# Kernel optimization log

Hardware: AMD Instinct MI355X
Metric: run time of the kernel (lower is better)

The kernel has to match this reference:

```python
import jax, jax.numpy as jnp
import numpy as np

N_NODES = 100000
N_EDGES = 1600000
NODE_DIM = 128
EDGE_DIM = 32
HIDDEN_DIM = 256


def _linear_params(key, fan_in, fan_out):
    kw, kb = jax.random.split(key)
    bound = 1.0 / np.sqrt(fan_in)
    W = jax.random.uniform(kw, (fan_in, fan_out), minval=-bound, maxval=bound, dtype=jnp.float32)
    b = jax.random.uniform(kb, (fan_out,), minval=-bound, maxval=bound, dtype=jnp.float32)
    return W, b


def setup_inputs() -> dict:
    key = jax.random.key(0)
    ks = jax.random.split(key, 8)
    x = jax.random.normal(ks[0], (N_NODES, NODE_DIM), dtype=jnp.float32)
    edge_index = jax.random.randint(ks[1], (2, N_EDGES), 0, N_NODES, dtype=jnp.int64)
    edge_attr = jax.random.normal(ks[2], (N_EDGES, EDGE_DIM), dtype=jnp.float32)
    congestion = jax.random.uniform(ks[3], (N_NODES,), dtype=jnp.float32)
    msg_in = 2 * NODE_DIM + EDGE_DIM + 1
    mW1, mb1 = _linear_params(ks[4], msg_in, HIDDEN_DIM)
    mW2, mb2 = _linear_params(ks[5], HIDDEN_DIM, NODE_DIM)
    uW1, ub1 = _linear_params(ks[6], 2 * NODE_DIM, HIDDEN_DIM)
    uW2, ub2 = _linear_params(ks[7], HIDDEN_DIM, NODE_DIM)
    return {
        "x": x, "edge_index": edge_index, "edge_attr": edge_attr, "congestion": congestion,
        "mW1": mW1, "mb1": mb1, "mW2": mW2, "mb2": mb2,
        "uW1": uW1, "ub1": ub1, "uW2": uW2, "ub2": ub2,
    }


def reference(x, edge_index, edge_attr, congestion, mW1, mb1, mW2, mb2, uW1, ub1, uW2, ub2):
    src, dst = edge_index[0], edge_index[1]
    # gather node features and src congestion, concat along feature dim  [E, 2D+edge_dim+1]
    msg_in = jnp.concatenate(
        [x[src], x[dst], edge_attr, congestion[src][:, None]], axis=-1)
    h = jax.nn.relu(msg_in @ mW1 + mb1)          # [E, hidden]
    messages = h @ mW2 + mb2                     # [E, node_dim]
    # scatter_add messages into destination nodes  [N, node_dim]
    aggregated = jax.ops.segment_sum(messages, dst, num_segments=x.shape[0])
    upd_in = jnp.concatenate([x, aggregated], axis=-1)  # [N, 2*node_dim]
    h2 = jax.nn.relu(upd_in @ uW1 + ub1)
    x_new = h2 @ uW2 + ub2                       # [N, node_dim]
    return x_new
```

## Files before the change

kernel.cpp:

```cpp
#include <hip/hip_runtime.h>

#define E_TOTAL 1600000
#define NN 100000
#define D 128
#define ED 32
#define H 256

typedef __attribute__((ext_vector_type(8))) short s16x8;
typedef __attribute__((ext_vector_type(4))) short s16x4;
typedef __attribute__((ext_vector_type(4))) float f32x4;

#define MFMA(a, b, c) __builtin_amdgcn_mfma_f32_16x16x32_bf16((a), (b), (c), 0, 0, 0)

__device__ __forceinline__ short f2bf(float f) {
    unsigned u = __builtin_bit_cast(unsigned, f);
    u += 0x7fffu + ((u >> 16) & 1u);
    return (short)(u >> 16);
}
__device__ __forceinline__ float bf2f(short s) {
    return __builtin_bit_cast(float, ((unsigned)(unsigned short)s) << 16);
}

__device__ __forceinline__ void gll16(const void* g, void* l) {
    __builtin_amdgcn_global_load_lds(
        (const __attribute__((address_space(1))) void*)g,
        (__attribute__((address_space(3))) void*)l, 16, 0, 0);
}

__device__ __forceinline__ void swz_one(const float* __restrict__ W,
                                        short* __restrict__ out,
                                        int K, int N, int idx) {
    int j    = idx & 7;
    int lane = (idx >> 3) & 63;
    int rest = idx >> 9;
    int NT   = N >> 4;
    int nt   = rest % NT;
    int t    = rest / NT;
    int k    = t * 32 + (lane >> 4) * 8 + j;
    int col  = nt * 16 + (lane & 15);
    out[idx] = f2bf((k < K) ? W[k * N + col] : 0.f);
}

__global__ void k_prep(const float* __restrict__ x, short* __restrict__ xb,
                       const int* __restrict__ ei, int* __restrict__ cnt,
                       const float* __restrict__ mW1, short* __restrict__ W1s,
                       const float* __restrict__ mW2, short* __restrict__ W2s,
                       const float* __restrict__ uW1, short* __restrict__ U1s,
                       const float* __restrict__ uW2, short* __restrict__ U2s) {
    const int b = blockIdx.x;
    if (b < 12500) {
        int i = (b * 256 + threadIdx.x) * 4;
        if (i >= NN * D) return;
        f32x4 v = *(const f32x4*)(x + i);
        s16x4 o;
        o[0] = f2bf(v[0]); o[1] = f2bf(v[1]); o[2] = f2bf(v[2]); o[3] = f2bf(v[3]);
        *(s16x4*)(xb + i) = o;
    } else if (b < 18750) {
        int e = (b - 12500) * 256 + threadIdx.x;
        if (e < E_TOTAL) atomicAdd(&cnt[ei[E_TOTAL + e]], 1);
    } else {
        int idx = (b - 18750) * 256 + threadIdx.x;
        if (idx < 81920) { swz_one(mW1, W1s, 289, 256, idx); return; }
        idx -= 81920;
        if (idx < 32768) { swz_one(mW2, W2s, 256, 128, idx); return; }
        idx -= 32768;
        if (idx < 65536) { swz_one(uW1, U1s, 256, 256, idx); return; }
        idx -= 65536;
        if (idx < 32768) { swz_one(uW2, U2s, 256, 128, idx); }
    }
}

__global__ void k_scan1(int* __restrict__ cnt, int* __restrict__ psum, int n) {
    __shared__ int wsum[16];
    __shared__ int woff[16];
    const int tid = threadIdx.x, lane = tid & 63, wv = tid >> 6;
    int i = blockIdx.x * 1024 + tid;
    int v = (i < n) ? cnt[i] : 0;
    int s = v;
#pragma unroll
    for (int off = 1; off < 64; off <<= 1) {
        int u = __shfl_up(s, off, 64);
        if (lane >= off) s += u;
    }
    if (lane == 63) wsum[wv] = s;
    __syncthreads();
    if (wv == 0 && lane < 16) {
        int t = wsum[lane];
        int sc = t;
#pragma unroll
        for (int off = 1; off < 16; off <<= 1) {
            int u = __shfl_up(sc, off, 16);
            if (lane >= off) sc += u;
        }
        woff[lane] = sc - t;
    }
    __syncthreads();
    int excl = (s - v) + woff[wv];
    if (i < n) cnt[i] = excl;
    if (tid == 1023) psum[blockIdx.x] = excl + v;
}

__global__ void k_scan2(int* __restrict__ psum, int nb) {
    __shared__ int w0;
    const int tid = threadIdx.x, lane = tid & 63, wv = tid >> 6;
    int v = (tid < nb) ? psum[tid] : 0;
    int s = v;
#pragma unroll
    for (int off = 1; off < 64; off <<= 1) {
        int u = __shfl_up(s, off, 64);
        if (lane >= off) s += u;
    }
    if (wv == 0 && lane == 63) w0 = s;
    __syncthreads();
    int excl = (s - v) + (wv ? w0 : 0);
    if (tid < nb) psum[tid] = excl;
}

__global__ void k_scan3(const int* __restrict__ psum, int* __restrict__ cnt, int n) {
    int i = blockIdx.x * 1024 + threadIdx.x;
    if (i < n) cnt[i] += psum[blockIdx.x];
}

__global__ void k_perm(const int* __restrict__ ei, int* __restrict__ cursor,
                       int* __restrict__ perm, int2* __restrict__ srcdst) {
    int e = blockIdx.x * blockDim.x + threadIdx.x;
    if (e >= E_TOTAL) return;
    int s = ei[e], d = ei[E_TOTAL + e];
    int pos = atomicAdd(&cursor[d], 1);
    perm[pos] = e;
    srcdst[pos] = make_int2(s, d);
}

__global__ __launch_bounds__(512, 4)
void k_pre(const short* __restrict__ xb, const short* __restrict__ W1s,
           short* __restrict__ yd) {
    __shared__ char smem[32768];
    const int tid  = threadIdx.x;
    const int lane = tid & 63;
    const int w    = tid >> 6;
    const int eh   = w >> 2;
    const int cg   = w & 3;
    const int m    = lane & 15;
    const int q    = lane >> 4;
    const int r0   = blockIdx.x * 128;

    {
        int rowl = w * 16 + (lane >> 2);
        int grow = r0 + rowl;
        int gc   = grow < NN ? grow : 0;
        int kqs  = (lane & 3) ^ ((lane >> 3) & 3);
        const char* gx = (const char*)xb + (long)gc * 256 + kqs * 16;
#pragma unroll
        for (int t = 0; t < 4; t++)
            gll16(gx + t * 64, smem + t * 8192 + w * 1024);
    }
    __syncthreads();

    const int rdoff = m * 64 + ((q ^ ((m >> 1) & 3)) << 4);

    f32x4 acc[4][4];
#pragma unroll
    for (int mt = 0; mt < 4; mt++)
#pragma unroll
        for (int n = 0; n < 4; n++) acc[mt][n] = (f32x4){0.f, 0.f, 0.f, 0.f};

#pragma unroll
    for (int t = 0; t < 4; t++) {
        s16x8 b[4];
        const short* bw = W1s + ((4 + t) * 16 + cg * 4) * 512 + lane * 8;
#pragma unroll
        for (int n = 0; n < 4; n++) b[n] = *(const s16x8*)(bw + n * 512);
#pragma unroll
        for (int mt = 0; mt < 4; mt++) {
            s16x8 a = *(const s16x8*)(smem + t * 8192 + (eh * 4 + mt) * 1024 + rdoff);
#pragma unroll
            for (int n = 0; n < 4; n++) acc[mt][n] = MFMA(a, b[n], acc[mt][n]);
        }
    }

#pragma unroll
    for (int mt = 0; mt < 4; mt++)
#pragma unroll
        for (int r = 0; r < 4; r++) {
            int grow = r0 + eh * 64 + mt * 16 + q * 4 + r;
            if (grow < NN) {
#pragma unroll
                for (int n = 0; n < 4; n++)
                    yd[(long)grow * H + cg * 64 + n * 16 + m] = f2bf(acc[mt][n][r]);
            }
        }
}

__global__ __launch_bounds__(512, 4)
void k_edge(const short* __restrict__ xb, const int* __restrict__ perm,
            const int2* __restrict__ srcdst, const short* __restrict__ yd,
            const float* __restrict__ eattr, const float* __restrict__ cong,
            const short* __restrict__ W1s, const float* __restrict__ b1,
            const short* __restrict__ W2s, const float* __restrict__ b2,
            float* __restrict__ agg) {
    __shared__ char smem[67584];
    __shared__ int   dst_s[128];
    __shared__ short cong_s[128];

    const int tid  = threadIdx.x;
    const int lane = tid & 63;
    const int w    = tid >> 6;
    const int eh   = w >> 2;
    const int cg   = w & 3;
    const int m    = lane & 15;
    const int q    = lane >> 4;
    const int p0b  = blockIdx.x * 128;

    {
        int edge = w * 16 + (lane >> 2);
        int2 sd  = srcdst[p0b + edge];
        int kqs  = (lane & 3) ^ ((lane >> 3) & 3);
        const char* gx0 = (const char*)xb + (long)sd.x * 256 + kqs * 16;
#pragma unroll
        for (int t = 0; t < 4; t++)
            gll16(gx0 + t * 64, smem + t * 8192 + w * 1024);
        int ea = perm[p0b + edge];
        const float* ge = eattr + (long)ea * ED + kqs * 8;
        f32x4 e0 = *(const f32x4*)ge, e1 = *(const f32x4*)(ge + 4);
        s16x8 ev;
#pragma unroll
        for (int j = 0; j < 4; j++) { ev[j] = f2bf(e0[j]); ev[4 + j] = f2bf(e1[j]); }
        *(s16x8*)(smem + 4 * 8192 + w * 1024 + lane * 16) = ev;
        if (tid < 128) {
            int2 sd2 = srcdst[p0b + tid];
            dst_s[tid]  = sd2.y;
            cong_s[tid] = f2bf(cong[sd2.x]);
        }
    }
    __syncthreads();

    const int rdoff = m * 64 + ((q ^ ((m >> 1) & 3)) << 4);

    f32x4 acc[4][4];
#pragma unroll
    for (int mt = 0; mt < 4; mt++)
#pragma unroll
        for (int n = 0; n < 4; n++) acc[mt][n] = (f32x4){0.f, 0.f, 0.f, 0.f};

#pragma unroll
    for (int t = 0; t < 5; t++) {
        const int wt = (t < 4) ? t : 8;
        s16x8 b[4];
        const short* bw = W1s + (wt * 16 + cg * 4) * 512 + lane * 8;
#pragma unroll
        for (int n = 0; n < 4; n++) b[n] = *(const s16x8*)(bw + n * 512);
#pragma unroll
        for (int mt = 0; mt < 4; mt++) {
            s16x8 a = *(const s16x8*)(smem + t * 8192 + (eh * 4 + mt) * 1024 + rdoff);
#pragma unroll
            for (int n = 0; n < 4; n++) acc[mt][n] = MFMA(a, b[n], acc[mt][n]);
        }
    }
    {
        s16x8 b[4];
        const short* bw = W1s + (9 * 16 + cg * 4) * 512 + lane * 8;
#pragma unroll
        for (int n = 0; n < 4; n++) b[n] = *(const s16x8*)(bw + n * 512);
#pragma unroll
        for (int mt = 0; mt < 4; mt++) {
            s16x8 a = (s16x8){0, 0, 0, 0, 0, 0, 0, 0};
            short cv = cong_s[eh * 64 + mt * 16 + m];
            a[0] = (q == 0) ? cv : (short)0;
#pragma unroll
            for (int n = 0; n < 4; n++) acc[mt][n] = MFMA(a, b[n], acc[mt][n]);
        }
    }
    __syncthreads();

    {
        short* hb16 = (short*)smem;
#pragma unroll
        for (int mt = 0; mt < 4; mt++) {
#pragma unroll
            for (int r = 0; r < 4; r++) {
                int edge = eh * 64 + mt * 16 + q * 4 + r;
                int key  = (2 * q + (r >> 1)) & 3;
                const short* ydp = yd + (long)dst_s[edge] * H + cg * 64 + m;
#pragma unroll
                for (int n = 0; n < 4; n++) {
                    const int chunk = 2 * cg + (n >> 1);
                    const int srq   = (n & 1) * 2 + (m >> 3);
                    int phys = srq ^ key;
                    float v  = acc[mt][n][r] + b1[cg * 64 + n * 16 + m]
                             + bf2f(ydp[n * 16]);
                    hb16[chunk * 4096 + edge * 32 + phys * 8 + (m & 7)] =
                        f2bf(v > 0.f ? v : 0.f);
                }
            }
        }
    }
    __syncthreads();

    f32x4 acc2[4][2];
#pragma unroll
    for (int mt = 0; mt < 4; mt++) {
        acc2[mt][0] = (f32x4){0.f, 0.f, 0.f, 0.f};
        acc2[mt][1] = (f32x4){0.f, 0.f, 0.f, 0.f};
    }
#pragma unroll
    for (int t2 = 0; t2 < 8; t2++) {
        const short* bw = W2s + (t2 * 8 + cg * 2) * 512 + lane * 8;
        s16x8 b0  = *(const s16x8*)bw;
        s16x8 b1v = *(const s16x8*)(bw + 512);
#pragma unroll
        for (int mt = 0; mt < 4; mt++) {
            s16x8 a = *(const s16x8*)(smem + t2 * 8192 + (eh * 4 + mt) * 1024 + rdoff);
            acc2[mt][0] = MFMA(a, b0, acc2[mt][0]);
            acc2[mt][1] = MFMA(a, b1v, acc2[mt][1]);
        }
    }
    __syncthreads();

    {
        float (*mbuf)[132] = (float (*)[132])smem;
        float bb0 = b2[cg * 32 + m];
        float bb1 = b2[cg * 32 + 16 + m];
#pragma unroll
        for (int mt = 0; mt < 4; mt++)
#pragma unroll
            for (int r = 0; r < 4; r++) {
                int edge = eh * 64 + mt * 16 + q * 4 + r;
                mbuf[edge][cg * 32 + m]      = acc2[mt][0][r] + bb0;
                mbuf[edge][cg * 32 + 16 + m] = acc2[mt][1][r] + bb1;
            }
    }
    __syncthreads();

    {
        float (*mbuf)[132] = (float (*)[132])smem;
        const int qtr = tid >> 7, cc = tid & 127;
        float s = 0.f;
        int prev = dst_s[qtr * 32];
        for (int row = qtr * 32; row < qtr * 32 + 32; row++) {
            int dcur = dst_s[row];
            if (dcur != prev) {
                __hip_atomic_fetch_add(agg + (long)prev * D + cc, s,
                                       __ATOMIC_RELAXED, __HIP_MEMORY_SCOPE_AGENT);
                s = 0.f; prev = dcur;
            }
            s += mbuf[row][cc];
        }
        __hip_atomic_fetch_add(agg + (long)prev * D + cc, s,
                               __ATOMIC_RELAXED, __HIP_MEMORY_SCOPE_AGENT);
    }
}

__global__ __launch_bounds__(512, 4)
void k_node(const short* __restrict__ xb, const float* __restrict__ agg,
            const short* __restrict__ U1s, const float* __restrict__ b1,
            const short* __restrict__ U2s, const float* __restrict__ b2,
            float* __restrict__ out) {
    __shared__ char smem[65536];
    const int tid  = threadIdx.x;
    const int lane = tid & 63;
    const int w    = tid >> 6;
    const int eh   = w >> 2;
    const int cg   = w & 3;
    const int m    = lane & 15;
    const int q    = lane >> 4;
    const int r0   = blockIdx.x * 128;

    {
        int rowl = w * 16 + (lane >> 2);
        int grow = r0 + rowl;
        int gc   = grow < NN ? grow : 0;
        int kqs  = (lane & 3) ^ ((lane >> 3) & 3);
        const char* gx = (const char*)xb + (long)gc * 256 + kqs * 16;
#pragma unroll
        for (int t = 0; t < 4; t++)
            gll16(gx + t * 64, smem + t * 8192 + w * 1024);
        const float* ga = agg + (long)gc * D + kqs * 8;
#pragma unroll
        for (int t = 0; t < 4; t++) {
            f32x4 a0 = *(const f32x4*)(ga + t * 32);
            f32x4 a1 = *(const f32x4*)(ga + t * 32 + 4);
            s16x8 v;
#pragma unroll
            for (int j = 0; j < 4; j++) { v[j] = f2bf(a0[j]); v[4 + j] = f2bf(a1[j]); }
            *(s16x8*)(smem + (4 + t) * 8192 + w * 1024 + lane * 16) = v;
        }
    }
    __syncthreads();

    const int rdoff = m * 64 + ((q ^ ((m >> 1) & 3)) << 4);

    f32x4 acc[4][4];
#pragma unroll
    for (int mt = 0; mt < 4; mt++)
#pragma unroll
        for (int n = 0; n < 4; n++) acc[mt][n] = (f32x4){0.f, 0.f, 0.f, 0.f};

#pragma unroll
    for (int t = 0; t < 8; t++) {
        s16x8 b[4];
        const short* bw = U1s + (t * 16 + cg * 4) * 512 + lane * 8;
#pragma unroll
        for (int n = 0; n < 4; n++) b[n] = *(const s16x8*)(bw + n * 512);
#pragma unroll
        for (int mt = 0; mt < 4; mt++) {
            s16x8 a = *(const s16x8*)(smem + t * 8192 + (eh * 4 + mt) * 1024 + rdoff);
#pragma unroll
            for (int n = 0; n < 4; n++) acc[mt][n] = MFMA(a, b[n], acc[mt][n]);
        }
    }
    __syncthreads();

    {
        short* hb16 = (short*)smem;
#pragma unroll
        for (int n = 0; n < 4; n++) {
            const int chunk = 2 * cg + (n >> 1);
            const int srq   = (n & 1) * 2 + (m >> 3);
            const float bias = b1[cg * 64 + n * 16 + m];
#pragma unroll
            for (int mt = 0; mt < 4; mt++) {
#pragma unroll
                for (int r = 0; r < 4; r++) {
                    int row = eh * 64 + mt * 16 + q * 4 + r;
                    int key = (2 * q + (r >> 1)) & 3;
                    int phys = srq ^ key;
                    float v = acc[mt][n][r] + bias;
                    hb16[chunk * 4096 + row * 32 + phys * 8 + (m & 7)] =
                        f2bf(v > 0.f ? v : 0.f);
                }
            }
        }
    }
    __syncthreads();

    f32x4 acc2[4][2];
#pragma unroll
    for (int mt = 0; mt < 4; mt++) {
        acc2[mt][0] = (f32x4){0.f, 0.f, 0.f, 0.f};
        acc2[mt][1] = (f32x4){0.f, 0.f, 0.f, 0.f};
    }
#pragma unroll
    for (int t2 = 0; t2 < 8; t2++) {
        const short* bw = U2s + (t2 * 8 + cg * 2) * 512 + lane * 8;
        s16x8 b0  = *(const s16x8*)bw;
        s16x8 b1v = *(const s16x8*)(bw + 512);
#pragma unroll
        for (int mt = 0; mt < 4; mt++) {
            s16x8 a = *(const s16x8*)(smem + t2 * 8192 + (eh * 4 + mt) * 1024 + rdoff);
            acc2[mt][0] = MFMA(a, b0, acc2[mt][0]);
            acc2[mt][1] = MFMA(a, b1v, acc2[mt][1]);
        }
    }

    {
        float bb0 = b2[cg * 32 + m];
        float bb1 = b2[cg * 32 + 16 + m];
#pragma unroll
        for (int mt = 0; mt < 4; mt++)
#pragma unroll
            for (int r = 0; r < 4; r++) {
                int grow = r0 + eh * 64 + mt * 16 + q * 4 + r;
                if (grow < NN) {
                    out[(long)grow * D + cg * 32 + m]      = acc2[mt][0][r] + bb0;
                    out[(long)grow * D + cg * 32 + 16 + m] = acc2[mt][1][r] + bb1;
                }
            }
    }
}

extern "C" void kernel_launch(void* const* d_in, const int* in_sizes, int n_in,
                              void* d_out, int out_size, void* d_ws, size_t ws_size,
                              hipStream_t stream) {
    const float* x     = (const float*)d_in[0];
    const int*   ei    = (const int*)d_in[1];
    const float* eattr = (const float*)d_in[2];
    const float* cong  = (const float*)d_in[3];
    const float* mW1   = (const float*)d_in[4];
    const float* mb1   = (const float*)d_in[5];
    const float* mW2   = (const float*)d_in[6];
    const float* mb2   = (const float*)d_in[7];
    const float* uW1   = (const float*)d_in[8];
    const float* ub1   = (const float*)d_in[9];
    const float* uW2   = (const float*)d_in[10];
    const float* ub2   = (const float*)d_in[11];

    char* ws = (char*)d_ws;
    float* agg    = (float*)ws;
    short* xb     = (short*)(ws + 51200000);
    short* W1s    = (short*)(ws + 76800000);
    short* W2s    = (short*)(ws + 76963840);
    short* U1s    = (short*)(ws + 77029376);
    short* U2s    = (short*)(ws + 77160448);
    int*   cnt    = (int*)(ws + 77225984);
    int*   perm   = (int*)(ws + 77625984);
    int2*  srcdst = (int2*)(ws + 84025984);
    int*   psum   = (int*)(ws + 96825984);
    short* yd     = (short*)(ws + 96826496);

    hipMemsetAsync(agg, 0, (size_t)NN * D * sizeof(float), stream);
    hipMemsetAsync(cnt, 0, (size_t)NN * sizeof(int), stream);

    k_prep<<<19582, 256, 0, stream>>>(x, xb, ei, cnt,
                                      mW1, W1s, mW2, W2s, uW1, U1s, uW2, U2s);

    k_pre<<<(NN + 127) / 128, 512, 0, stream>>>(xb, W1s, yd);

    int nb = (NN + 1023) / 1024;
    k_scan1<<<nb, 1024, 0, stream>>>(cnt, psum, NN);
    k_scan2<<<1, 128, 0, stream>>>(psum, nb);
    k_scan3<<<nb, 1024, 0, stream>>>(psum, cnt, NN);
    k_perm<<<(E_TOTAL + 255) / 256, 256, 0, stream>>>(ei, cnt, perm, srcdst);

    k_edge<<<E_TOTAL / 128, 512, 0, stream>>>(xb, perm, srcdst, yd, eattr, cong,
                                              W1s, mb1, W2s, mb2, agg);
    k_node<<<(NN + 127) / 128, 512, 0, stream>>>(xb, agg, U1s, ub1, U2s, ub2,
                                                 (float*)d_out);
}
```

Baseline: 1.047 ms.

## Precompute per-node src projection of first message layer, gather it per edge

The x[src] @ W1 part of the message MLP's first layer is now computed once per node in k_pre, alongside the existing dst projection, and written to a new ys buffer. k_edge no longer loads x[src] rows into LDS or runs those four MFMA k-steps. It instead gathers 4-element bf16 chunks of ys[src] and yd[dst] per edge, with output layouts permuted for vectorized stores and loads. This removes most of the per-edge first-layer FLOPs and the x gather, at the cost of a per-node pre-GEMM pass, an extra 51 MB workspace buffer, and bf16 rounding of the src partial sum.

```diff
diff --git a/kernel.cpp b/kernel.cpp
--- a/kernel.cpp
+++ b/kernel.cpp
@@ -133,7 +133,7 @@
 
 __global__ __launch_bounds__(512, 4)
 void k_pre(const short* __restrict__ xb, const short* __restrict__ W1s,
-           short* __restrict__ yd) {
+           short* __restrict__ ys, short* __restrict__ yd) {
     __shared__ char smem[32768];
     const int tid  = threadIdx.x;
     const int lane = tid & 63;
@@ -158,48 +158,52 @@
 
     const int rdoff = m * 64 + ((q ^ ((m >> 1) & 3)) << 4);
 
-    f32x4 acc[4][4];
-#pragma unroll
-    for (int mt = 0; mt < 4; mt++)
-#pragma unroll
-        for (int n = 0; n < 4; n++) acc[mt][n] = (f32x4){0.f, 0.f, 0.f, 0.f};
-
-#pragma unroll
-    for (int t = 0; t < 4; t++) {
-        s16x8 b[4];
-        const short* bw = W1s + ((4 + t) * 16 + cg * 4) * 512 + lane * 8;
-#pragma unroll
-        for (int n = 0; n < 4; n++) b[n] = *(const s16x8*)(bw + n * 512);
-#pragma unroll
-        for (int mt = 0; mt < 4; mt++) {
-            s16x8 a = *(const s16x8*)(smem + t * 8192 + (eh * 4 + mt) * 1024 + rdoff);
-#pragma unroll
-            for (int n = 0; n < 4; n++) acc[mt][n] = MFMA(a, b[n], acc[mt][n]);
-        }
-    }
-
-#pragma unroll
-    for (int mt = 0; mt < 4; mt++)
-#pragma unroll
-        for (int r = 0; r < 4; r++) {
-            int grow = r0 + eh * 64 + mt * 16 + q * 4 + r;
-            if (grow < NN) {
-#pragma unroll
-                for (int n = 0; n < 4; n++)
-                    yd[(long)grow * H + cg * 64 + n * 16 + m] = f2bf(acc[mt][n][r]);
-            }
-        }
+#pragma unroll
+    for (int pass = 0; pass < 2; pass++) {
+        f32x4 acc[4][4];
+#pragma unroll
+        for (int mt = 0; mt < 4; mt++)
+#pragma unroll
+            for (int n = 0; n < 4; n++) acc[mt][n] = (f32x4){0.f, 0.f, 0.f, 0.f};
+#pragma unroll
+        for (int t = 0; t < 4; t++) {
+            s16x8 b[4];
+            const short* bw = W1s + ((pass * 4 + t) * 16 + cg * 4) * 512 + lane * 8;
+#pragma unroll
+            for (int n = 0; n < 4; n++) b[n] = *(const s16x8*)(bw + n * 512);
+#pragma unroll
+            for (int mt = 0; mt < 4; mt++) {
+                s16x8 a = *(const s16x8*)(smem + t * 8192 + (eh * 4 + mt) * 1024 + rdoff);
+#pragma unroll
+                for (int n = 0; n < 4; n++) acc[mt][n] = MFMA(a, b[n], acc[mt][n]);
+            }
+        }
+        short* out = pass ? yd : ys;
+#pragma unroll
+        for (int mt = 0; mt < 4; mt++)
+#pragma unroll
+            for (int r = 0; r < 4; r++) {
+                int grow = r0 + eh * 64 + mt * 16 + q * 4 + r;
+                if (grow < NN) {
+                    s16x4 o;
+#pragma unroll
+                    for (int n = 0; n < 4; n++) o[n] = f2bf(acc[mt][n][r]);
+                    *(s16x4*)(out + (long)grow * 256 + (cg * 16 + m) * 4) = o;
+                }
+            }
+    }
 }
 
 __global__ __launch_bounds__(512, 4)
-void k_edge(const short* __restrict__ xb, const int* __restrict__ perm,
-            const int2* __restrict__ srcdst, const short* __restrict__ yd,
+void k_edge(const int* __restrict__ perm, const int2* __restrict__ srcdst,
+            const short* __restrict__ ys, const short* __restrict__ yd,
             const float* __restrict__ eattr, const float* __restrict__ cong,
             const short* __restrict__ W1s, const float* __restrict__ b1,
             const short* __restrict__ W2s, const float* __restrict__ b2,
             float* __restrict__ agg) {
-    __shared__ char smem[67584];
+    __shared__ char smem[73728];
     __shared__ int   dst_s[128];
+    __shared__ int   src_s[128];
     __shared__ short cong_s[128];
 
     const int tid  = threadIdx.x;
@@ -213,22 +217,18 @@
 
     {
         int edge = w * 16 + (lane >> 2);
-        int2 sd  = srcdst[p0b + edge];
         int kqs  = (lane & 3) ^ ((lane >> 3) & 3);
-        const char* gx0 = (const char*)xb + (long)sd.x * 256 + kqs * 16;
-#pragma unroll
-        for (int t = 0; t < 4; t++)
-            gll16(gx0 + t * 64, smem + t * 8192 + w * 1024);
         int ea = perm[p0b + edge];
         const float* ge = eattr + (long)ea * ED + kqs * 8;
         f32x4 e0 = *(const f32x4*)ge, e1 = *(const f32x4*)(ge + 4);
         s16x8 ev;
 #pragma unroll
         for (int j = 0; j < 4; j++) { ev[j] = f2bf(e0[j]); ev[4 + j] = f2bf(e1[j]); }
-        *(s16x8*)(smem + 4 * 8192 + w * 1024 + lane * 16) = ev;
+        *(s16x8*)(smem + w * 1024 + lane * 16) = ev;
         if (tid < 128) {
             int2 sd2 = srcdst[p0b + tid];
             dst_s[tid]  = sd2.y;
+            src_s[tid]  = sd2.x;
             cong_s[tid] = f2bf(cong[sd2.x]);
         }
     }
@@ -242,16 +242,14 @@
 #pragma unroll
         for (int n = 0; n < 4; n++) acc[mt][n] = (f32x4){0.f, 0.f, 0.f, 0.f};
 
-#pragma unroll
-    for (int t = 0; t < 5; t++) {
-        const int wt = (t < 4) ? t : 8;
+    {
         s16x8 b[4];
-        const short* bw = W1s + (wt * 16 + cg * 4) * 512 + lane * 8;
+        const short* bw = W1s + (8 * 16 + cg * 4) * 512 + lane * 8;
 #pragma unroll
         for (int n = 0; n < 4; n++) b[n] = *(const s16x8*)(bw + n * 512);
 #pragma unroll
         for (int mt = 0; mt < 4; mt++) {
-            s16x8 a = *(const s16x8*)(smem + t * 8192 + (eh * 4 + mt) * 1024 + rdoff);
+            s16x8 a = *(const s16x8*)(smem + (eh * 4 + mt) * 1024 + rdoff);
 #pragma unroll
             for (int n = 0; n < 4; n++) acc[mt][n] = MFMA(a, b[n], acc[mt][n]);
         }
@@ -270,25 +268,34 @@
             for (int n = 0; n < 4; n++) acc[mt][n] = MFMA(a, b[n], acc[mt][n]);
         }
     }
-    __syncthreads();
-
-    {
-        short* hb16 = (short*)smem;
+
+    {
+        short* hb16 = (short*)(smem + 8192);
+        float b1c[4];
+#pragma unroll
+        for (int n = 0; n < 4; n++) b1c[n] = b1[cg * 64 + n * 16 + m];
+        const int qoff = (cg * 16 + m) * 4;
 #pragma unroll
         for (int mt = 0; mt < 4; mt++) {
+            s16x4 ysv[4], ydv[4];
 #pragma unroll
             for (int r = 0; r < 4; r++) {
-                int edge = eh * 64 + mt * 16 + q * 4 + r;
-                int key  = (2 * q + (r >> 1)) & 3;
-                const short* ydp = yd + (long)dst_s[edge] * H + cg * 64 + m;
+                int e = eh * 64 + mt * 16 + q * 4 + r;
+                ysv[r] = *(const s16x4*)(ys + (long)src_s[e] * 256 + qoff);
+                ydv[r] = *(const s16x4*)(yd + (long)dst_s[e] * 256 + qoff);
+            }
+#pragma unroll
+            for (int r = 0; r < 4; r++) {
+                int e = eh * 64 + mt * 16 + q * 4 + r;
+                int key = (2 * q + (r >> 1)) & 3;
 #pragma unroll
                 for (int n = 0; n < 4; n++) {
                     const int chunk = 2 * cg + (n >> 1);
                     const int srq   = (n & 1) * 2 + (m >> 3);
                     int phys = srq ^ key;
-                    float v  = acc[mt][n][r] + b1[cg * 64 + n * 16 + m]
-                             + bf2f(ydp[n * 16]);
-                    hb16[chunk * 4096 + edge * 32 + phys * 8 + (m & 7)] =
+                    float v = acc[mt][n][r] + b1c[n]
+                            + bf2f(ysv[r][n]) + bf2f(ydv[r][n]);
+                    hb16[chunk * 4096 + e * 32 + phys * 8 + (m & 7)] =
                         f2bf(v > 0.f ? v : 0.f);
                 }
             }
@@ -309,7 +316,8 @@
         s16x8 b1v = *(const s16x8*)(bw + 512);
 #pragma unroll
         for (int mt = 0; mt < 4; mt++) {
-            s16x8 a = *(const s16x8*)(smem + t2 * 8192 + (eh * 4 + mt) * 1024 + rdoff);
+            s16x8 a = *(const s16x8*)(smem + 8192 + t2 * 8192
+                                      + (eh * 4 + mt) * 1024 + rdoff);
             acc2[mt][0] = MFMA(a, b0, acc2[mt][0]);
             acc2[mt][1] = MFMA(a, b1v, acc2[mt][1]);
         }
@@ -496,6 +504,7 @@
     int2*  srcdst = (int2*)(ws + 84025984);
     int*   psum   = (int*)(ws + 96825984);
     short* yd     = (short*)(ws + 96826496);
+    short* ys     = (short*)(ws + 148026496);
 
     hipMemsetAsync(agg, 0, (size_t)NN * D * sizeof(float), stream);
     hipMemsetAsync(cnt, 0, (size_t)NN * sizeof(int), stream);
@@ -503,7 +512,7 @@
     k_prep<<<19582, 256, 0, stream>>>(x, xb, ei, cnt,
                                       mW1, W1s, mW2, W2s, uW1, U1s, uW2, U2s);
 
-    k_pre<<<(NN + 127) / 128, 512, 0, stream>>>(xb, W1s, yd);
+    k_pre<<<(NN + 127) / 128, 512, 0, stream>>>(xb, W1s, ys, yd);
 
     int nb = (NN + 1023) / 1024;
     k_scan1<<<nb, 1024, 0, stream>>>(cnt, psum, NN);
@@ -511,7 +520,7 @@
     k_scan3<<<nb, 1024, 0, stream>>>(psum, cnt, NN);
     k_perm<<<(E_TOTAL + 255) / 256, 256, 0, stream>>>(ei, cnt, perm, srcdst);
 
-    k_edge<<<E_TOTAL / 128, 512, 0, stream>>>(xb, perm, srcdst, yd, eattr, cong,
+    k_edge<<<E_TOTAL / 128, 512, 0, stream>>>(perm, srcdst, ys, yd, eattr, cong,
                                               W1s, mb1, W2s, mb2, agg);
     k_node<<<(NN + 127) / 128, 512, 0, stream>>>(xb, agg, U1s, ub1, U2s, ub2,
                                                  (float*)d_out);
```

Result: faster. 925.3 us (-11.6%).
